# Performance work log

Hardware: AMD Instinct MI355X
Metric: run time of the kernel (lower is better)

## Reference

```python
import jax, jax.numpy as jnp
import numpy as np

NEG_INF = -1e9
LEAKY_SLOPE = 0.2


def setup_inputs() -> dict:
    key = jax.random.key(0)
    k1, k2, k3, k4, k5 = jax.random.split(key, 5)
    B, N, F_in, F_out = 8, 2048, 256, 256
    x = jax.random.normal(k1, (B, N, F_in), dtype=jnp.float32)
    adj = jax.random.randint(k2, (B, N, N), 0, 2, dtype=jnp.int32)
    W = jax.random.normal(k3, (F_out, F_in), dtype=jnp.float32) * 0.05
    a_src = jax.random.normal(k4, (F_out,), dtype=jnp.float32) * 0.05
    a_dst = jax.random.normal(k5, (F_out,), dtype=jnp.float32) * 0.05
    return {"x": x, "adj": adj, "W": W, "a_src": a_src, "a_dst": a_dst}


def reference(x, adj, W, a_src, a_dst):
    # h: (B, N, F_out)
    h = jnp.einsum("bnf,of->bno", x, W)
    # a([h_i ; h_j]) == h_i @ a_src + h_j @ a_dst  (avoids O(N^2, 2F) concat)
    s_src = h @ a_src  # (B, N) score contribution of row node i
    s_dst = h @ a_dst  # (B, N) score contribution of col node j
    e = s_src[:, :, None] + s_dst[:, None, :]  # (B, N, N)
    e = jax.nn.leaky_relu(e, negative_slope=LEAKY_SLOPE)
    e = jnp.where(adj == 0, jnp.float32(NEG_INF), e)
    alpha = jax.nn.softmax(e, axis=-1)  # dropout is identity in eval mode
    h_prime = jnp.einsum("bij,bjo->bio", alpha, h)
    return h_prime
```

## Files before the change

kernel.cpp:

```cpp
#include <hip/hip_runtime.h>
#include <hip/hip_bf16.h>
#include <cstdint>
#include <cstddef>

typedef __attribute__((ext_vector_type(8))) short short8;
typedef __attribute__((ext_vector_type(4))) short short4v;
typedef __attribute__((ext_vector_type(4))) float floatx4;
typedef unsigned short ushort_t;

#define LOG2E 1.44269504088896340736f

__device__ __forceinline__ unsigned short f2bf(float f) {
    unsigned u = __float_as_uint(f);
    u += 0x7FFFu + ((u >> 16) & 1u);
    return (unsigned short)(u >> 16);
}
__device__ __forceinline__ float bf2f(unsigned short s) {
    return __uint_as_float(((unsigned)s) << 16);
}

__global__ __launch_bounds__(256) void wprep(const float* __restrict__ W,
                                             ushort_t* __restrict__ Wb) {
    int t = blockIdx.x * 256 + threadIdx.x;
    float4 v = ((const float4*)W)[t];
    short4v s;
    s[0] = (short)f2bf(v.x); s[1] = (short)f2bf(v.y);
    s[2] = (short)f2bf(v.z); s[3] = (short)f2bf(v.w);
    ((short4v*)Wb)[t] = s;
}

__global__ __launch_bounds__(256) void gemm_h(const float* __restrict__ x,
                                              const ushort_t* __restrict__ Wb,
                                              ushort_t* __restrict__ hT,
                                              const float* __restrict__ a_src,
                                              const float* __restrict__ a_dst,
                                              float* __restrict__ s_src,
                                              float* __restrict__ s_dst) {
    const int tid = threadIdx.x;
    const int w = tid >> 6, lane = tid & 63;
    const int q = lane >> 4, t16 = lane & 15;

    __shared__ ushort_t wt[256][72];

    const int jrow = blockIdx.x * 64 + w * 16 + t16;
    const float* xr = x + (size_t)jrow * 256 + q * 8;
    short8 af[8];
#pragma unroll
    for (int kb = 0; kb < 8; ++kb) {
        float4 v0 = *(const float4*)(xr + kb * 32);
        float4 v1 = *(const float4*)(xr + kb * 32 + 4);
        short8 a;
        a[0] = (short)f2bf(v0.x); a[1] = (short)f2bf(v0.y);
        a[2] = (short)f2bf(v0.z); a[3] = (short)f2bf(v0.w);
        a[4] = (short)f2bf(v1.x); a[5] = (short)f2bf(v1.y);
        a[6] = (short)f2bf(v1.z); a[7] = (short)f2bf(v1.w);
        af[kb] = a;
    }

    floatx4 acc[16] = {};
#pragma unroll
    for (int kp = 0; kp < 4; ++kp) {
        if (kp) __syncthreads();
#pragma unroll
        for (int r = 0; r < 8; ++r) {
            int G = tid + 256 * r;
            int row = G >> 3, g = G & 7;
            int4 wv = *(const int4*)(Wb + (size_t)row * 256 + kp * 64 + g * 8);
            *(int4*)(&wt[row][g * 8]) = wv;
        }
        __syncthreads();
#pragma unroll
        for (int ks = 0; ks < 2; ++ks) {
#pragma unroll
            for (int ct = 0; ct < 16; ++ct) {
                short8 bf = *(const short8*)(&wt[ct * 16 + t16][ks * 32 + q * 8]);
                acc[ct] = __builtin_amdgcn_mfma_f32_16x16x32_bf16(af[kp * 2 + ks], bf, acc[ct], 0, 0, 0);
            }
        }
    }

    const int jbase = blockIdx.x * 64 + w * 16 + q * 4;
    const int b = jbase >> 11, jj = jbase & 2047;
#pragma unroll
    for (int ct = 0; ct < 16; ++ct) {
        const int o = ct * 16 + t16;
        short4v sv;
        sv[0] = (short)f2bf(acc[ct][0]);
        sv[1] = (short)f2bf(acc[ct][1]);
        sv[2] = (short)f2bf(acc[ct][2]);
        sv[3] = (short)f2bf(acc[ct][3]);
        *(short4v*)(hT + ((size_t)b * 256 + o) * 2048 + jj) = sv;
    }

    float psv[4] = {}, pdv[4] = {};
#pragma unroll
    for (int ct = 0; ct < 16; ++ct) {
        const int o = ct * 16 + t16;
        float as = a_src[o], ad = a_dst[o];
#pragma unroll
        for (int r = 0; r < 4; ++r) {
            psv[r] = __fmaf_rn(acc[ct][r], as, psv[r]);
            pdv[r] = __fmaf_rn(acc[ct][r], ad, pdv[r]);
        }
    }
#pragma unroll
    for (int m = 1; m < 16; m <<= 1) {
#pragma unroll
        for (int r = 0; r < 4; ++r) {
            psv[r] += __shfl_xor(psv[r], m);
            pdv[r] += __shfl_xor(pdv[r], m);
        }
    }
    if (t16 == 0) {
#pragma unroll
        for (int r = 0; r < 4; ++r) {
            s_src[jbase + r] = psv[r];
            s_dst[jbase + r] = pdv[r];
        }
    }
}

__global__ __launch_bounds__(1024) void attn(const ushort_t* __restrict__ hT,
                                             const int* __restrict__ adj,
                                             const float* __restrict__ s_src,
                                             const float* __restrict__ s_dst,
                                             float* __restrict__ out) {
    const int tid = threadIdx.x;
    const int w = tid >> 6;
    const int lane = tid & 63;
    const int q = lane >> 4, t16 = lane & 15;
    const int b = blockIdx.x;
    const int i0 = blockIdx.y * 64;

    __shared__ ushort_t hts[2][256][40];
    __shared__ ushort_t ps[2][64][40];
    __shared__ float sdl[2048];
    __shared__ float lred[64][16];
    __shared__ float rll[64];

    const float* sdb = s_dst + (size_t)b * 2048;
    {
        int idx = tid * 2;
        float2 v = *(const float2*)(sdb + idx);
        v.x *= LOG2E; v.y *= LOG2E;
        *(float2*)(&sdl[idx]) = v;
    }

    const int prow = lane;
    const float si = s_src[(size_t)b * 2048 + i0 + prow] * LOG2E;
    const int* adjr = adj + ((size_t)b * 2048 + i0 + prow) * 2048 + w * 2;

    const int hrow = tid >> 2, hseg = tid & 3;
    const ushort_t* hTg = hT + ((size_t)b * 256 + hrow) * 2048 + hseg * 8;

    const int osub = (w & 3) * 64, ih = (w >> 2) * 16;

    floatx4 acc[4] = {};
    float lsum = 0.f;
    int4 hreg;
    int2 a2;

    hreg = *(const int4*)(hTg);
    a2 = *(const int2*)(adjr);
    __syncthreads();

    for (int c = 0; c < 64; ++c) {
        const int buf = c & 1;
        *(int4*)(&hts[buf][hrow][hseg * 8]) = hreg;
        {
            float2 sd = *(const float2*)(&sdl[c * 32 + w * 2]);
            float t0 = si + sd.x;
            float t1 = si + sd.y;
            float l0 = fmaxf(t0, 0.2f * t0);
            float l1 = fmaxf(t1, 0.2f * t1);
            float p0 = __builtin_amdgcn_exp2f(l0);
            float p1 = __builtin_amdgcn_exp2f(l1);
            p0 = (a2.x != 0) ? p0 : 0.0f;
            p1 = (a2.y != 0) ? p1 : 0.0f;
            unsigned short u0 = f2bf(p0);
            unsigned short u1 = f2bf(p1);
            lsum += bf2f(u0) + bf2f(u1);
            unsigned pw = (unsigned)u0 | ((unsigned)u1 << 16);
            *(unsigned*)(&ps[buf][prow][w * 2]) = pw;
        }
        if (c < 63) {
            hreg = *(const int4*)(hTg + (c + 1) * 32);
            a2 = *(const int2*)(adjr + (size_t)(c + 1) * 32);
        }
        __syncthreads();
        short8 bf = *(const short8*)(&ps[buf][ih + t16][q * 8]);
#pragma unroll
        for (int ct = 0; ct < 4; ++ct) {
            short8 af = *(const short8*)(&hts[buf][osub + ct * 16 + t16][q * 8]);
            acc[ct] = __builtin_amdgcn_mfma_f32_16x16x32_bf16(af, bf, acc[ct], 0, 0, 0);
        }
    }

    lred[prow][w] = lsum;
    __syncthreads();
    if (tid < 64) {
        float s = 0.f;
#pragma unroll
        for (int k = 0; k < 16; ++k) s += lred[tid][k];
        rll[tid] = (s > 0.f) ? 1.0f / s : 0.0f;
    }
    __syncthreads();

    {
        const int i = ih + t16;
        const float rl = rll[i];
        float* orow = out + ((size_t)b * 2048 + i0 + i) * 256 + osub + q * 4;
#pragma unroll
        for (int ct = 0; ct < 4; ++ct) {
            floatx4 v = acc[ct] * rl;
            *(floatx4*)(orow + ct * 16) = v;
        }
    }
}

extern "C" void kernel_launch(void* const* d_in, const int* in_sizes, int n_in,
                              void* d_out, int out_size, void* d_ws, size_t ws_size,
                              hipStream_t stream) {
    const float* x     = (const float*)d_in[0];
    const int*   adj   = (const int*)d_in[1];
    const float* W     = (const float*)d_in[2];
    const float* a_src = (const float*)d_in[3];
    const float* a_dst = (const float*)d_in[4];
    float* out = (float*)d_out;

    char* ws = (char*)d_ws;
    ushort_t* hT = (ushort_t*)ws;
    float* s_src = (float*)(ws + (size_t)8 * 1024 * 1024);
    float* s_dst = s_src + 16384;
    ushort_t* Wb = (ushort_t*)(s_dst + 16384);

    wprep<<<64, 256, 0, stream>>>(W, Wb);
    gemm_h<<<256, 256, 0, stream>>>(x, Wb, hT, a_src, a_dst, s_src, s_dst);
    attn<<<dim3(8, 32), 1024, 0, stream>>>(hT, adj, s_src, s_dst, out);
}
```

Baseline: 246.9 us.

## Use 32x32 MFMA in attention, remap P rows, widen projection GEMM blocks

The attention kernel moves from 16x16x32 MFMA tiles to a single 32x32x16 accumulator per wave. It also remaps the probability-producing threads so each row's adjacency reads are contiguous across 16 lanes, and replaces the shared-memory row-sum reduction with a shuffle reduction. The next chunk's loads are issued before the exp computation to overlap latency. The projection GEMM now runs 1024 threads per block split across output columns, with an added shared-memory reduction for the score vectors, trading a barrier for more waves and fewer accumulators per wave.

```diff
diff --git a/kernel.cpp b/kernel.cpp
--- a/kernel.cpp
+++ b/kernel.cpp
@@ -6,6 +6,7 @@
 typedef __attribute__((ext_vector_type(8))) short short8;
 typedef __attribute__((ext_vector_type(4))) short short4v;
 typedef __attribute__((ext_vector_type(4))) float floatx4;
+typedef __attribute__((ext_vector_type(16))) float floatx16;
 typedef unsigned short ushort_t;
 
 #define LOG2E 1.44269504088896340736f
@@ -29,20 +30,22 @@
     ((short4v*)Wb)[t] = s;
 }
 
-__global__ __launch_bounds__(256) void gemm_h(const float* __restrict__ x,
-                                              const ushort_t* __restrict__ Wb,
-                                              ushort_t* __restrict__ hT,
-                                              const float* __restrict__ a_src,
-                                              const float* __restrict__ a_dst,
-                                              float* __restrict__ s_src,
-                                              float* __restrict__ s_dst) {
+__global__ __launch_bounds__(1024) void gemm_h(const float* __restrict__ x,
+                                               const ushort_t* __restrict__ Wb,
+                                               ushort_t* __restrict__ hT,
+                                               const float* __restrict__ a_src,
+                                               const float* __restrict__ a_dst,
+                                               float* __restrict__ s_src,
+                                               float* __restrict__ s_dst) {
     const int tid = threadIdx.x;
     const int w = tid >> 6, lane = tid & 63;
     const int q = lane >> 4, t16 = lane & 15;
+    const int jg = w >> 2, og = w & 3;
 
     __shared__ ushort_t wt[256][72];
-
-    const int jrow = blockIdx.x * 64 + w * 16 + t16;
+    __shared__ float sred[2][4][64];
+
+    const int jrow = blockIdx.x * 64 + jg * 16 + t16;
     const float* xr = x + (size_t)jrow * 256 + q * 8;
     short8 af[8];
 #pragma unroll
@@ -57,13 +60,13 @@
         af[kb] = a;
     }
 
-    floatx4 acc[16] = {};
+    floatx4 acc[4] = {};
 #pragma unroll
     for (int kp = 0; kp < 4; ++kp) {
         if (kp) __syncthreads();
 #pragma unroll
-        for (int r = 0; r < 8; ++r) {
-            int G = tid + 256 * r;
+        for (int r = 0; r < 2; ++r) {
+            int G = tid + 1024 * r;
             int row = G >> 3, g = G & 7;
             int4 wv = *(const int4*)(Wb + (size_t)row * 256 + kp * 64 + g * 8);
             *(int4*)(&wt[row][g * 8]) = wv;
@@ -72,18 +75,18 @@
 #pragma unroll
         for (int ks = 0; ks < 2; ++ks) {
 #pragma unroll
-            for (int ct = 0; ct < 16; ++ct) {
-                short8 bf = *(const short8*)(&wt[ct * 16 + t16][ks * 32 + q * 8]);
+            for (int ct = 0; ct < 4; ++ct) {
+                short8 bf = *(const short8*)(&wt[og * 64 + ct * 16 + t16][ks * 32 + q * 8]);
                 acc[ct] = __builtin_amdgcn_mfma_f32_16x16x32_bf16(af[kp * 2 + ks], bf, acc[ct], 0, 0, 0);
             }
         }
     }
 
-    const int jbase = blockIdx.x * 64 + w * 16 + q * 4;
+    const int jbase = blockIdx.x * 64 + jg * 16 + q * 4;
     const int b = jbase >> 11, jj = jbase & 2047;
 #pragma unroll
-    for (int ct = 0; ct < 16; ++ct) {
-        const int o = ct * 16 + t16;
+    for (int ct = 0; ct < 4; ++ct) {
+        const int o = og * 64 + ct * 16 + t16;
         short4v sv;
         sv[0] = (short)f2bf(acc[ct][0]);
         sv[1] = (short)f2bf(acc[ct][1]);
@@ -94,8 +97,8 @@
 
     float psv[4] = {}, pdv[4] = {};
 #pragma unroll
-    for (int ct = 0; ct < 16; ++ct) {
-        const int o = ct * 16 + t16;
+    for (int ct = 0; ct < 4; ++ct) {
+        const int o = og * 64 + ct * 16 + t16;
         float as = a_src[o], ad = a_dst[o];
 #pragma unroll
         for (int r = 0; r < 4; ++r) {
@@ -114,9 +117,16 @@
     if (t16 == 0) {
 #pragma unroll
         for (int r = 0; r < 4; ++r) {
-            s_src[jbase + r] = psv[r];
-            s_dst[jbase + r] = pdv[r];
-        }
+            sred[0][og][jg * 16 + q * 4 + r] = psv[r];
+            sred[1][og][jg * 16 + q * 4 + r] = pdv[r];
+        }
+    }
+    __syncthreads();
+    if (tid < 64) {
+        float ss = sred[0][0][tid] + sred[0][1][tid] + sred[0][2][tid] + sred[0][3][tid];
+        float dd = sred[1][0][tid] + sred[1][1][tid] + sred[1][2][tid] + sred[1][3][tid];
+        s_src[blockIdx.x * 64 + tid] = ss;
+        s_dst[blockIdx.x * 64 + tid] = dd;
     }
 }
 
@@ -128,15 +138,14 @@
     const int tid = threadIdx.x;
     const int w = tid >> 6;
     const int lane = tid & 63;
-    const int q = lane >> 4, t16 = lane & 15;
+    const int l5 = lane & 31, hi = lane >> 5;
     const int b = blockIdx.x;
     const int i0 = blockIdx.y * 64;
 
     __shared__ ushort_t hts[2][256][40];
     __shared__ ushort_t ps[2][64][40];
     __shared__ float sdl[2048];
-    __shared__ float lred[64][16];
-    __shared__ float rll[64];
+    __shared__ float rls[64];
 
     const float* sdb = s_dst + (size_t)b * 2048;
     {
@@ -146,16 +155,17 @@
         *(float2*)(&sdl[idx]) = v;
     }
 
-    const int prow = lane;
-    const float si = s_src[(size_t)b * 2048 + i0 + prow] * LOG2E;
-    const int* adjr = adj + ((size_t)b * 2048 + i0 + prow) * 2048 + w * 2;
+    const int ip = w * 4 + (lane >> 4);
+    const int jp = lane & 15;
+    const float si = s_src[(size_t)b * 2048 + i0 + ip] * LOG2E;
+    const int* adjr = adj + ((size_t)b * 2048 + i0 + ip) * 2048 + jp * 2;
 
     const int hrow = tid >> 2, hseg = tid & 3;
     const ushort_t* hTg = hT + ((size_t)b * 256 + hrow) * 2048 + hseg * 8;
 
-    const int osub = (w & 3) * 64, ih = (w >> 2) * 16;
-
-    floatx4 acc[4] = {};
+    const int osub = (w & 7) * 32, ih = (w >> 3) * 32;
+
+    floatx16 acc = {};
     float lsum = 0.f;
     int4 hreg;
     int2 a2;
@@ -167,53 +177,53 @@
     for (int c = 0; c < 64; ++c) {
         const int buf = c & 1;
         *(int4*)(&hts[buf][hrow][hseg * 8]) = hreg;
+        int2 ac = a2;
+        if (c < 63) {
+            hreg = *(const int4*)(hTg + (c + 1) * 32);
+            a2 = *(const int2*)(adjr + (size_t)(c + 1) * 32);
+        }
         {
-            float2 sd = *(const float2*)(&sdl[c * 32 + w * 2]);
+            float2 sd = *(const float2*)(&sdl[c * 32 + jp * 2]);
             float t0 = si + sd.x;
             float t1 = si + sd.y;
             float l0 = fmaxf(t0, 0.2f * t0);
             float l1 = fmaxf(t1, 0.2f * t1);
             float p0 = __builtin_amdgcn_exp2f(l0);
             float p1 = __builtin_amdgcn_exp2f(l1);
-            p0 = (a2.x != 0) ? p0 : 0.0f;
-            p1 = (a2.y != 0) ? p1 : 0.0f;
+            p0 = (ac.x != 0) ? p0 : 0.0f;
+            p1 = (ac.y != 0) ? p1 : 0.0f;
             unsigned short u0 = f2bf(p0);
             unsigned short u1 = f2bf(p1);
             lsum += bf2f(u0) + bf2f(u1);
-            unsigned pw = (unsigned)u0 | ((unsigned)u1 << 16);
-            *(unsigned*)(&ps[buf][prow][w * 2]) = pw;
-        }
-        if (c < 63) {
-            hreg = *(const int4*)(hTg + (c + 1) * 32);
-            a2 = *(const int2*)(adjr + (size_t)(c + 1) * 32);
+            *(unsigned*)(&ps[buf][ip][jp * 2]) = (unsigned)u0 | ((unsigned)u1 << 16);
         }
         __syncthreads();
-        short8 bf = *(const short8*)(&ps[buf][ih + t16][q * 8]);
-#pragma unroll
-        for (int ct = 0; ct < 4; ++ct) {
-            short8 af = *(const short8*)(&hts[buf][osub + ct * 16 + t16][q * 8]);
-            acc[ct] = __builtin_amdgcn_mfma_f32_16x16x32_bf16(af, bf, acc[ct], 0, 0, 0);
-        }
-    }
-
-    lred[prow][w] = lsum;
+#pragma unroll
+        for (int ks = 0; ks < 2; ++ks) {
+            short8 afr = *(const short8*)(&hts[buf][osub + l5][ks * 16 + hi * 8]);
+            short8 bfr = *(const short8*)(&ps[buf][ih + l5][ks * 16 + hi * 8]);
+            acc = __builtin_amdgcn_mfma_f32_32x32x16_bf16(afr, bfr, acc, 0, 0, 0);
+        }
+    }
+
+#pragma unroll
+    for (int m = 1; m < 16; m <<= 1) lsum += __shfl_xor(lsum, m);
+    if (jp == 0) rls[ip] = lsum;
     __syncthreads();
-    if (tid < 64) {
-        float s = 0.f;
-#pragma unroll
-        for (int k = 0; k < 16; ++k) s += lred[tid][k];
-        rll[tid] = (s > 0.f) ? 1.0f / s : 0.0f;
-    }
-    __syncthreads();
 
     {
-        const int i = ih + t16;
-        const float rl = rll[i];
-        float* orow = out + ((size_t)b * 2048 + i0 + i) * 256 + osub + q * 4;
-#pragma unroll
-        for (int ct = 0; ct < 4; ++ct) {
-            floatx4 v = acc[ct] * rl;
-            *(floatx4*)(orow + ct * 16) = v;
+        const int i = ih + l5;
+        const float s = rls[i];
+        const float rl = (s > 0.f) ? 1.0f / s : 0.0f;
+        float* orow = out + ((size_t)b * 2048 + i0 + i) * 256 + osub;
+#pragma unroll
+        for (int rq = 0; rq < 4; ++rq) {
+            floatx4 v;
+            v[0] = acc[rq * 4 + 0] * rl;
+            v[1] = acc[rq * 4 + 1] * rl;
+            v[2] = acc[rq * 4 + 2] * rl;
+            v[3] = acc[rq * 4 + 3] * rl;
+            *(floatx4*)(orow + rq * 8 + hi * 4) = v;
         }
     }
 }
@@ -235,6 +245,6 @@
     ushort_t* Wb = (ushort_t*)(s_dst + 16384);
 
     wprep<<<64, 256, 0, stream>>>(W, Wb);
-    gemm_h<<<256, 256, 0, stream>>>(x, Wb, hT, a_src, a_dst, s_src, s_dst);
+    gemm_h<<<256, 1024, 0, stream>>>(x, Wb, hT, a_src, a_dst, s_src, s_dst);
     attn<<<dim3(8, 32), 1024, 0, stream>>>(hT, adj, s_src, s_dst, out);
 }
```

After: 249.0 us. No clear change (+0.9%).
